# Kernel optimization log

Hardware: AMD Instinct MI355X
Metric: run time of the kernel (lower is better)

The kernel has to match this reference:

```python
import jax, jax.numpy as jnp
import numpy as np

B, D, STRIDE, OUT = 8192, 1024, 16, 64
L = D // STRIDE


def setup_inputs() -> dict:
    key = jax.random.key(0)
    kx, kw, kb = jax.random.split(key, 3)
    x = jax.random.normal(kx, (B, D), dtype=jnp.float32)
    # Stacked per-layer Dense kernels: layer i only sees features j < i*STRIDE.
    # Glorot-ish scale; masked entries are zeroed in reference() (faithful: they
    # don't exist in the original per-layer kernels).
    W = jax.random.normal(kw, (L, D, OUT), dtype=jnp.float32) * 0.02
    b = jax.random.normal(kb, (L, OUT), dtype=jnp.float32) * 0.02
    return {"x": x, "W": W, "b": b}


def reference(x, W, b):
    # Original: tf.stack([Dense_i(x[..., :i*stride]) for i in range(L)], -2)
    # Equivalent single causal-masked batched matmul.
    Lx, Dx, Ox = W.shape
    stride = Dx // Lx
    # mask[l, d] = 1 if feature d is visible to layer l (d < l*stride)
    mask = (jnp.arange(Dx)[None, :] < (jnp.arange(Lx) * stride)[:, None]).astype(W.dtype)
    Wm = W * mask[:, :, None]                      # [L, D, O]
    out = jnp.einsum("bd,ldo->blo", x, Wm) + b    # [B, L, O]
    return out
```

## Files before the change

kernel.cpp:

```cpp
#include <hip/hip_runtime.h>
#include <hip/hip_bf16.h>
#include <stdint.h>

#define BROWS 8192
#define DDIM  1024
#define LDIM  64
#define ODIM  64
#define NDIM  4096
#define KSTRIDE 16

typedef __attribute__((ext_vector_type(8))) short bf16x8;
typedef __attribute__((ext_vector_type(4))) float f32x4;
typedef __attribute__((ext_vector_type(8))) unsigned short u16x8;

static __device__ __forceinline__ unsigned short f2bf(float f) {
    union { float f; uint32_t u; } v; v.f = f;
    uint32_t r = 0x7FFFu + ((v.u >> 16) & 1u);
    return (unsigned short)((v.u + r) >> 16);
}

static __device__ __forceinline__ void async16(const void* g, void* l) {
    __builtin_amdgcn_global_load_lds(
        (const __attribute__((address_space(1))) void*)g,
        (__attribute__((address_space(3))) void*)l, 16, 0, 0);
}

__global__ __launch_bounds__(256) void prep_kernel(const float* __restrict__ x,
                                                   const float* __restrict__ W,
                                                   unsigned short* __restrict__ xb,
                                                   unsigned short* __restrict__ wbt) {
    const int bid = blockIdx.x;
    if (bid < 1024) {
        __shared__ float tile[64][65];
        const int l  = bid >> 4;
        const int d0 = (bid & 15) << 6;
        const int t  = threadIdx.x;
        {
            const int dd = t >> 2;
            const int o4 = (t & 3) << 4;
            const float* src = W + ((size_t)((l << 10) + d0 + dd) << 6) + o4;
            #pragma unroll
            for (int j = 0; j < 4; ++j) {
                float4 v = reinterpret_cast<const float4*>(src)[j];
                tile[dd][o4 + 4 * j + 0] = v.x;
                tile[dd][o4 + 4 * j + 1] = v.y;
                tile[dd][o4 + 4 * j + 2] = v.z;
                tile[dd][o4 + 4 * j + 3] = v.w;
            }
        }
        __syncthreads();
        {
            const int o    = t >> 2;
            const int dloc = (t & 3) << 4;
            const int kmax = l * KSTRIDE;
            unsigned short* dst = wbt + ((size_t)((l << 6) + o) << 10) + d0 + dloc;
            u16x8 r0, r1;
            #pragma unroll
            for (int j = 0; j < 8; ++j) {
                int da = d0 + dloc + j;
                int db = da + 8;
                r0[j] = (da < kmax) ? f2bf(tile[dloc + j][o])     : (unsigned short)0;
                r1[j] = (db < kmax) ? f2bf(tile[dloc + 8 + j][o]) : (unsigned short)0;
            }
            *reinterpret_cast<u16x8*>(dst)     = r0;
            *reinterpret_cast<u16x8*>(dst + 8) = r1;
        }
    } else {
        int i = (bid - 1024) * 256 + threadIdx.x;
        const float4* xf = reinterpret_cast<const float4*>(x);
        float4 v0 = xf[2 * i];
        float4 v1 = xf[2 * i + 1];
        u16x8 r;
        r[0] = f2bf(v0.x); r[1] = f2bf(v0.y); r[2] = f2bf(v0.z); r[3] = f2bf(v0.w);
        r[4] = f2bf(v1.x); r[5] = f2bf(v1.y); r[6] = f2bf(v1.z); r[7] = f2bf(v1.w);
        reinterpret_cast<u16x8*>(xb)[i] = r;
    }
}

__global__ __launch_bounds__(256, 2) void ar_gemm_kernel(
        const unsigned short* __restrict__ xb,
        const unsigned short* __restrict__ wbt,
        const float* __restrict__ bias,
        float* __restrict__ out) {
    __shared__ unsigned short As[128 * 32];
    __shared__ unsigned short Bs[128 * 32];

    const int s  = blockIdx.x >> 8;
    const int i  = blockIdx.x & 255;
    const int bm = ((s & 3) << 4) + (i & 15);
    const int bn = ((s < 4) ? 16 : 0) + 15 - (i >> 4);
    const int tid  = threadIdx.x;
    const int lane = tid & 63;
    const int wave = tid >> 6;
    const int wr   = wave >> 1;
    const int wc   = wave & 1;

    const int nkt = ((2 * bn + 1) * KSTRIDE + 31) >> 5;

    const int rc = lane >> 2;
    const int cb = (lane & 3) << 4;
    const char* gA0 = (const char*)xb  + ((size_t)(bm * 128 + (2 * wave + 0) * 16 + rc) * 2048) + cb;
    const char* gA1 = (const char*)xb  + ((size_t)(bm * 128 + (2 * wave + 1) * 16 + rc) * 2048) + cb;
    const char* gB0 = (const char*)wbt + ((size_t)(bn * 128 + (2 * wave + 0) * 16 + rc) * 2048) + cb;
    const char* gB1 = (const char*)wbt + ((size_t)(bn * 128 + (2 * wave + 1) * 16 + rc) * 2048) + cb;
    char* lA0 = (char*)As + (2 * wave + 0) * 1024;
    char* lA1 = (char*)As + (2 * wave + 1) * 1024;
    char* lB0 = (char*)Bs + (2 * wave + 0) * 1024;
    char* lB1 = (char*)Bs + (2 * wave + 1) * 1024;

    const int aoff = ((wr << 6) + (lane & 15)) * 64 + ((lane >> 4) << 4);
    const int boff = ((wc << 6) + (lane & 15)) * 64 + ((lane >> 4) << 4);

    f32x4 acc[4][4];
    #pragma unroll
    for (int m = 0; m < 4; ++m)
        #pragma unroll
        for (int n = 0; n < 4; ++n)
            acc[m][n] = (f32x4)(0.f);

    for (int kt = 0; kt < nkt; ++kt) {
        const int kb = kt << 6;
        async16(gA0 + kb, lA0);
        async16(gA1 + kb, lA1);
        async16(gB0 + kb, lB0);
        async16(gB1 + kb, lB1);
        __syncthreads();
        bf16x8 a[4], b[4];
        #pragma unroll
        for (int m = 0; m < 4; ++m)
            a[m] = *reinterpret_cast<const bf16x8*>((const char*)As + aoff + m * 1024);
        #pragma unroll
        for (int n = 0; n < 4; ++n)
            b[n] = *reinterpret_cast<const bf16x8*>((const char*)Bs + boff + n * 1024);
        #pragma unroll
        for (int m = 0; m < 4; ++m)
            #pragma unroll
            for (int n = 0; n < 4; ++n)
                acc[m][n] = __builtin_amdgcn_mfma_f32_16x16x32_bf16(a[m], b[n], acc[m][n], 0, 0, 0);
        __syncthreads();
    }

    const int crow = (bm << 7) + (wr << 6) + ((lane >> 4) << 2);
    const int ccol = (bn << 7) + (wc << 6) + (lane & 15);
    float bv[4];
    #pragma unroll
    for (int n = 0; n < 4; ++n) bv[n] = bias[ccol + n * 16];
    #pragma unroll
    for (int m = 0; m < 4; ++m)
        #pragma unroll
        for (int n = 0; n < 4; ++n)
            #pragma unroll
            for (int j = 0; j < 4; ++j)
                out[(size_t)(crow + m * 16 + j) * NDIM + ccol + n * 16] = acc[m][n][j] + bv[n];
}

__global__ __launch_bounds__(256) void naive_kernel(const float* __restrict__ x,
                                                    const float* __restrict__ W,
                                                    const float* __restrict__ bias,
                                                    float* __restrict__ out) {
    size_t idx = (size_t)blockIdx.x * 256 + threadIdx.x;
    if (idx >= (size_t)BROWS * NDIM) return;
    int m = (int)(idx >> 12);
    int n = (int)(idx & 4095);
    int l = n >> 6;
    int o = n & 63;
    int kmax = l * KSTRIDE;
    float s = bias[n];
    const float* xr = x + (size_t)m * DDIM;
    const float* wp = W + ((size_t)l << 16) + o;
    for (int d = 0; d < kmax; ++d) s += xr[d] * wp[(size_t)d << 6];
    out[idx] = s;
}

extern "C" void kernel_launch(void* const* d_in, const int* in_sizes, int n_in,
                              void* d_out, int out_size, void* d_ws, size_t ws_size,
                              hipStream_t stream) {
    const float* x = (const float*)d_in[0];
    const float* W = (const float*)d_in[1];
    const float* b = (const float*)d_in[2];
    float* out = (float*)d_out;

    const size_t need = ((size_t)BROWS * DDIM + (size_t)NDIM * DDIM) * sizeof(unsigned short);
    if (ws_size < need) {
        int total = BROWS * NDIM;
        naive_kernel<<<(total + 255) / 256, 256, 0, stream>>>(x, W, b, out);
        return;
    }
    unsigned short* xbuf = (unsigned short*)d_ws;
    unsigned short* wbt  = xbuf + (size_t)BROWS * DDIM;

    prep_kernel<<<5120, 256, 0, stream>>>(x, W, xbuf, wbt);
    ar_gemm_kernel<<<2048, 256, 0, stream>>>(xbuf, wbt, b, out);
}
```

Measured before the change: 64.24 us.

## Use 256x128 tiles with 8 waves and double-buffered LDS prefetch

Grows the GEMM block tile from 128x128 to 256x128 with 512 threads (8 waves, each still computing 64x64). LDS is now double-buffered so the async global-to-LDS load of the next K tile overlaps the MFMAs on the current one, and one barrier per iteration is removed. The K-trip count becomes bn+1, relying on the causal mask. The aim is to hide load latency and reuse each B tile across more rows, at the cost of 48KB LDS per block and half as many blocks, which may reduce occupancy.

```diff
diff --git a/kernel.cpp b/kernel.cpp
--- a/kernel.cpp
+++ b/kernel.cpp
@@ -77,39 +77,31 @@
     }
 }
 
-__global__ __launch_bounds__(256, 2) void ar_gemm_kernel(
+__global__ __launch_bounds__(512, 2) void ar_gemm_kernel(
         const unsigned short* __restrict__ xb,
         const unsigned short* __restrict__ wbt,
         const float* __restrict__ bias,
         float* __restrict__ out) {
-    __shared__ unsigned short As[128 * 32];
-    __shared__ unsigned short Bs[128 * 32];
+    __shared__ char lds[49152];
 
     const int s  = blockIdx.x >> 8;
     const int i  = blockIdx.x & 255;
-    const int bm = ((s & 3) << 4) + (i & 15);
-    const int bn = ((s < 4) ? 16 : 0) + 15 - (i >> 4);
+    const int bm = ((s & 1) << 4) + (i & 15);
+    const int bn = ((s < 2) ? 16 : 0) + 15 - (i >> 4);
     const int tid  = threadIdx.x;
     const int lane = tid & 63;
-    const int wave = tid >> 6;
-    const int wr   = wave >> 1;
-    const int wc   = wave & 1;
+    const int wid  = tid >> 6;
+    const int wm   = wid >> 1;
+    const int wn   = wid & 1;
 
-    const int nkt = ((2 * bn + 1) * KSTRIDE + 31) >> 5;
+    const int nkt = bn + 1;
 
-    const int rc = lane >> 2;
-    const int cb = (lane & 3) << 4;
-    const char* gA0 = (const char*)xb  + ((size_t)(bm * 128 + (2 * wave + 0) * 16 + rc) * 2048) + cb;
-    const char* gA1 = (const char*)xb  + ((size_t)(bm * 128 + (2 * wave + 1) * 16 + rc) * 2048) + cb;
-    const char* gB0 = (const char*)wbt + ((size_t)(bn * 128 + (2 * wave + 0) * 16 + rc) * 2048) + cb;
-    const char* gB1 = (const char*)wbt + ((size_t)(bn * 128 + (2 * wave + 1) * 16 + rc) * 2048) + cb;
-    char* lA0 = (char*)As + (2 * wave + 0) * 1024;
-    char* lA1 = (char*)As + (2 * wave + 1) * 1024;
-    char* lB0 = (char*)Bs + (2 * wave + 0) * 1024;
-    char* lB1 = (char*)Bs + (2 * wave + 1) * 1024;
+    const int cb = (tid & 3) << 4;
+    const char* gA = (const char*)xb  + ((size_t)((bm << 8) + (tid >> 2)) << 11) + cb;
+    const char* gB = (const char*)wbt + ((size_t)((bn << 7) + (tid >> 2)) << 11) + cb;
 
-    const int aoff = ((wr << 6) + (lane & 15)) * 64 + ((lane >> 4) << 4);
-    const int boff = ((wc << 6) + (lane & 15)) * 64 + ((lane >> 4) << 4);
+    const int aoff = ((wm << 6) + (lane & 15)) * 64 + ((lane >> 4) << 4);
+    const int boff = 16384 + ((wn << 6) + (lane & 15)) * 64 + ((lane >> 4) << 4);
 
     f32x4 acc[4][4];
     #pragma unroll
@@ -118,20 +110,28 @@
         for (int n = 0; n < 4; ++n)
             acc[m][n] = (f32x4)(0.f);
 
-    for (int kt = 0; kt < nkt; ++kt) {
-        const int kb = kt << 6;
-        async16(gA0 + kb, lA0);
-        async16(gA1 + kb, lA1);
-        async16(gB0 + kb, lB0);
-        async16(gB1 + kb, lB1);
-        __syncthreads();
+    auto stage = [&](int t, int p) {
+        const int kb = (t < nkt ? t : nkt - 1) << 6;
+        char* l = lds + p * 24576 + tid * 16;
+        async16(gA + kb, l);
+        async16(gA + ((size_t)128 << 11) + kb, l + 8192);
+        async16(gB + kb, l + 16384);
+    };
+
+    stage(0, 0);
+    __syncthreads();
+
+    for (int t = 0; t < nkt; ++t) {
+        const int p = t & 1;
+        stage(t + 1, p ^ 1);
+        const char* pb = lds + p * 24576;
         bf16x8 a[4], b[4];
         #pragma unroll
         for (int m = 0; m < 4; ++m)
-            a[m] = *reinterpret_cast<const bf16x8*>((const char*)As + aoff + m * 1024);
+            a[m] = *reinterpret_cast<const bf16x8*>(pb + aoff + m * 1024);
         #pragma unroll
         for (int n = 0; n < 4; ++n)
-            b[n] = *reinterpret_cast<const bf16x8*>((const char*)Bs + boff + n * 1024);
+            b[n] = *reinterpret_cast<const bf16x8*>(pb + boff + n * 1024);
         #pragma unroll
         for (int m = 0; m < 4; ++m)
             #pragma unroll
@@ -140,8 +140,8 @@
         __syncthreads();
     }
 
-    const int crow = (bm << 7) + (wr << 6) + ((lane >> 4) << 2);
-    const int ccol = (bn << 7) + (wc << 6) + (lane & 15);
+    const int crow = (bm << 8) + (wm << 6) + ((lane >> 4) << 2);
+    const int ccol = (bn << 7) + (wn << 6) + (lane & 15);
     float bv[4];
     #pragma unroll
     for (int n = 0; n < 4; ++n) bv[n] = bias[ccol + n * 16];
@@ -190,5 +190,5 @@
     unsigned short* wbt  = xbuf + (size_t)BROWS * DDIM;
 
     prep_kernel<<<5120, 256, 0, stream>>>(x, W, xbuf, wbt);
-    ar_gemm_kernel<<<2048, 256, 0, stream>>>(xbuf, wbt, b, out);
+    ar_gemm_kernel<<<1024, 512, 0, stream>>>(xbuf, wbt, b, out);
 }
```

After: 63.99 us. No clear change (-0.4%).
